# Optimization experiments

Hardware: AMD Instinct MI355X
Metric: run time of the kernel (lower is better)

The kernel has to match this reference:

```python
import jax, jax.numpy as jnp
import numpy as np
from jax import lax

KS = 5            # patch kernel size
STRIDE = 4        # patch stride / scale ratio
SHIFTS = (2, 2)   # roll shifts before patch extraction
SOFTMAX_SCALE = 10.0
MID_CH = 64
BAND_HS = 8


def same_pad(x, k, s):
    """TensorFlow-style SAME padding for kernel k, stride s (NCHW)."""
    H, W = x.shape[-2], x.shape[-1]
    oh, ow = -(-H // s), -(-W // s)
    ph = max(0, (oh - 1) * s + k - H)
    pw = max(0, (ow - 1) * s + k - W)
    return jnp.pad(x, ((0, 0), (0, 0), (ph // 2, ph - ph // 2), (pw // 2, pw - pw // 2)))


def extract_patches(x, k, s, shifts):
    """torch.nn.Unfold equivalent with SAME padding and roll -> [N, L, C, k, k]."""
    x = same_pad(x, k, s)
    x = jnp.roll(x, shifts[0], axis=2)
    x = jnp.roll(x, shifts[1], axis=3)
    p = lax.conv_general_dilated_patches(
        x, (k, k), (s, s), 'VALID', dimension_numbers=('NCHW', 'OIHW', 'NCHW'))
    N, _, Hn, Wn = p.shape
    C = x.shape[1]
    # channel ordering is (C, kh, kw) channel-slowest, matching torch unfold
    return p.reshape(N, C, k, k, Hn * Wn).transpose(0, 4, 1, 2, 3)


def conv3(x, w, b):
    """3x3 conv, padding=1, bias + LeakyReLU(0.01) (BasicBlock)."""
    y = lax.conv_general_dilated(x, w, (1, 1), [(1, 1), (1, 1)],
                                 dimension_numbers=('NCHW', 'OIHW', 'NCHW'))
    return jax.nn.leaky_relu(y + b[None, :, None, None], 0.01)


def setup_inputs() -> dict:
    key = jax.random.key(0)
    ks = jax.random.split(key, 11)
    f32 = jnp.float32
    return {
        'ms':   jax.random.normal(ks[0], (2, BAND_HS, 96, 96), f32),
        'pan':  jax.random.normal(ks[1], (2, 1, 384, 384), f32),
        'pan2': jax.random.normal(ks[2], (2, 1, 96, 96), f32),
        'wq': jax.random.normal(ks[3], (MID_CH, 1, 3, 3), f32) * 0.1,
        'bq': jax.random.normal(ks[4], (MID_CH,), f32) * 0.02,
        'wk': jax.random.normal(ks[5], (MID_CH, 1, 3, 3), f32) * 0.1,
        'bk': jax.random.normal(ks[6], (MID_CH,), f32) * 0.02,
        'wv': jax.random.normal(ks[7], (BAND_HS, BAND_HS, 3, 3), f32) * 0.1,
        'bv': jax.random.normal(ks[8], (BAND_HS,), f32) * 0.02,
        'wr': jax.random.normal(ks[9], (BAND_HS, BAND_HS, 3, 3), f32) * 0.1,
        'br': jax.random.normal(ks[10], (BAND_HS,), f32) * 0.02,
    }


def reference(ms, pan, pan2, wq, bq, wk, bk, wv, bv, wr, br):
    k_fea = conv3(pan2, wk, bk)                       # [N, mid, h, w]
    q_fea = conv3(pan, wq, bq)                        # [N, mid, H, W]
    v_fea = conv3(ms, wv, bv)                         # [N, band, h, w]

    k_patch = extract_patches(k_fea, KS, STRIDE, SHIFTS)  # [N, L, mid, ks, ks]
    v_patch = extract_patches(v_fea, KS, STRIDE, SHIFTS)  # [N, L, band, ks, ks]

    def attend(q, kp, vp):
        # q: [mid, H, W]; kp: [L, mid, ks, ks]; vp: [L, band, ks, ks]
        norms = jnp.sqrt(jnp.sum(kp * kp, axis=(1, 2, 3)))      # per-patch L2 norms
        k0 = kp / jnp.max(norms)                                # global-max normalization
        q0 = same_pad(q[None], KS, STRIDE)                      # [1, mid, Hp, Wp]
        scores = lax.conv_general_dilated(
            q0, k0, (STRIDE, STRIDE), 'VALID',
            dimension_numbers=('NCHW', 'OIHW', 'NCHW'))          # [1, L, H', W']
        attn = jax.nn.softmax(scores * SOFTMAX_SCALE, axis=1)
        # conv_transpose2d(attn, vp, stride) == dilated conv with flipped, transposed kernel
        wT = jnp.flip(vp, (2, 3)).transpose(1, 0, 2, 3)          # [band, L, ks, ks]
        out = lax.conv_general_dilated(
            attn, wT, (1, 1), [(KS - 1, KS - 1)] * 2,
            lhs_dilation=(STRIDE, STRIDE),
            dimension_numbers=('NCHW', 'OIHW', 'NCHW'))          # [1, band, Ho, Wo]
        return out[0] / 6.0

    res = jax.vmap(attend)(q_fea, k_patch, v_patch)   # [N, band, Ho, Wo]
    return conv3(res, wr, br)
```

## Files before the change

kernel.cpp:

```cpp
#include <hip/hip_runtime.h>
#include <math.h>


typedef _Float16 f16;
typedef _Float16 f16x8 __attribute__((ext_vector_type(8)));
typedef float f32x4 __attribute__((ext_vector_type(4)));

namespace csa {
constexpr int NB   = 2;
constexpr int MID  = 64;
constexpr int BAND = 8;
constexpr int HK   = 96;
constexpr int HQ   = 384;
constexpr int HQP  = 385;
constexpr int XI   = 97;
constexpr int LN   = 24;
constexpr int L    = 576;
constexpr int LP   = 640;
constexpr int PS   = 96 * 96;
constexpr int KDIM = MID * 25;
constexpr int VDIM = BAND * 25;
constexpr int MV   = 256;
constexpr int HO   = 385;
constexpr size_t QPSN = (size_t)4 * HQP * XI * MID;

constexpr size_t align256(size_t x) { return (x + 255) & ~(size_t)255; }
constexpr size_t OFF_QPS  = 0;
constexpr size_t OFF_KCL  = align256(OFF_QPS + (size_t)NB*QPSN*2);
constexpr size_t OFF_VFEA = align256(OFF_KCL + (size_t)NB*HK*HK*MID*2);
constexpr size_t OFF_N2   = align256(OFF_VFEA + (size_t)NB*BAND*HK*HK*4);
constexpr size_t OFF_SC   = align256(OFF_N2   + (size_t)NB*L*4);
constexpr size_t OFF_KM   = align256(OFF_SC   + 256);
constexpr size_t OFF_VT   = align256(OFF_KM   + (size_t)NB*LP*KDIM*2);
constexpr size_t OFF_ST   = align256(OFF_VT   + (size_t)NB*MV*L*2);
constexpr size_t OFF_AT   = align256(OFF_ST   + (size_t)NB*PS*LP*4);
constexpr size_t OFF_D    = align256(OFF_AT   + (size_t)NB*PS*L*2);
constexpr size_t OFF_RES  = align256(OFF_D    + (size_t)NB*MV*PS*4);
}
using namespace csa;

__global__ __launch_bounds__(256) void csa_convq_ps(
    const float* __restrict__ in, const float* __restrict__ w,
    const float* __restrict__ b, f16* __restrict__ out) {
  int id = blockIdx.x * 256 + threadIdx.x;
  int total = NB * 4 * HQP * XI;
  if (id >= total) return;
  int xi = id % XI;
  int t = id / XI;
  int yp = t % HQP;
  t /= HQP;
  int f = t % 4;
  int n = t / 4;
  int xp = 4 * xi + f;
  f16* op = out + (size_t)id * MID;
  if (yp >= HQ || xp >= HQ) {
    f16x8 z = {0, 0, 0, 0, 0, 0, 0, 0};
#pragma unroll
    for (int c8 = 0; c8 < 8; ++c8) *(f16x8*)(op + c8 * 8) = z;
    return;
  }
  const float* ip = in + (size_t)n * HQ * HQ;
  float p[9];
#pragma unroll
  for (int dy = 0; dy < 3; ++dy)
#pragma unroll
    for (int dx = 0; dx < 3; ++dx) {
      int yy = yp + dy - 1, xx = xp + dx - 1;
      p[dy * 3 + dx] = (yy >= 0 && yy < HQ && xx >= 0 && xx < HQ)
                           ? ip[(size_t)yy * HQ + xx] : 0.f;
    }
#pragma unroll
  for (int c8 = 0; c8 < 8; ++c8) {
    f16x8 o;
#pragma unroll
    for (int e = 0; e < 8; ++e) {
      int co = c8 * 8 + e;
      float acc = b[co];
#pragma unroll
      for (int k = 0; k < 9; ++k) acc = fmaf(p[k], w[co * 9 + k], acc);
      o[e] = (f16)(acc > 0.f ? acc : 0.01f * acc);
    }
    *(f16x8*)(op + c8 * 8) = o;
  }
}

__global__ __launch_bounds__(256) void csa_conv_cl(
    const float* __restrict__ in, const float* __restrict__ w,
    const float* __restrict__ b, f16* __restrict__ out, int H) {
  int id = blockIdx.x * 256 + threadIdx.x;
  int total = NB * H * H;
  if (id >= total) return;
  int x = id % H;
  int t = id / H;
  int y = t % H;
  int n = t / H;
  f16* op = out + (size_t)id * MID;
  const float* ip = in + (size_t)n * H * H;
  float p[9];
#pragma unroll
  for (int dy = 0; dy < 3; ++dy)
#pragma unroll
    for (int dx = 0; dx < 3; ++dx) {
      int yy = y + dy - 1, xx = x + dx - 1;
      p[dy * 3 + dx] = (yy >= 0 && yy < H && xx >= 0 && xx < H)
                           ? ip[(size_t)yy * H + xx] : 0.f;
    }
#pragma unroll
  for (int c8 = 0; c8 < 8; ++c8) {
    f16x8 o;
#pragma unroll
    for (int e = 0; e < 8; ++e) {
      int co = c8 * 8 + e;
      float acc = b[co];
#pragma unroll
      for (int k = 0; k < 9; ++k) acc = fmaf(p[k], w[co * 9 + k], acc);
      o[e] = (f16)(acc > 0.f ? acc : 0.01f * acc);
    }
    *(f16x8*)(op + c8 * 8) = o;
  }
}

__global__ __launch_bounds__(256) void csa_conv3_8x8(
    const float* __restrict__ in, const float* __restrict__ w,
    const float* __restrict__ b, float* __restrict__ out, int H, int W) {
  int id = blockIdx.x * 256 + threadIdx.x;
  int total = NB * H * W;
  if (id >= total) return;
  int x = id % W;
  int t = id / W;
  int y = t % H;
  int n = t / H;
  const float* ip = in + (size_t)n * BAND * H * W;
  float p[BAND][9];
#pragma unroll
  for (int ci = 0; ci < BAND; ++ci)
#pragma unroll
    for (int dy = 0; dy < 3; ++dy)
#pragma unroll
      for (int dx = 0; dx < 3; ++dx) {
        int yy = y + dy - 1, xx = x + dx - 1;
        p[ci][dy * 3 + dx] = (yy >= 0 && yy < H && xx >= 0 && xx < W)
                                 ? ip[((size_t)ci * H + yy) * W + xx] : 0.f;
      }
  float* op = out + ((size_t)n * BAND * H + y) * W + x;
  for (int co = 0; co < BAND; ++co) {
    float acc = b[co];
#pragma unroll
    for (int ci = 0; ci < BAND; ++ci)
#pragma unroll
      for (int k = 0; k < 9; ++k)
        acc = fmaf(p[ci][k], w[(co * BAND + ci) * 9 + k], acc);
    acc = acc > 0.f ? acc : 0.01f * acc;
    op[(size_t)co * H * W] = acc;
  }
}

__global__ __launch_bounds__(256) void csa_build_patches(
    const f16* __restrict__ kcl, const float* __restrict__ v_fea,
    f16* __restrict__ Kmat, f16* __restrict__ Vt, float* __restrict__ n2) {
  int blk = blockIdx.x;
  int n = blk / LP;
  int l = blk % LP;
  int tid = threadIdx.x;
  f16* krow = Kmat + ((size_t)n * LP + l) * KDIM;
  if (l >= L) {
    f16x8 z = {0, 0, 0, 0, 0, 0, 0, 0};
    for (int ch = tid; ch < 200; ch += 256) *(f16x8*)(krow + ch * 8) = z;
    return;
  }
  int i = l / LN, j = l % LN;
  const f16* kn = kcl + (size_t)n * HK * HK * MID;
  float ss = 0.f;
  for (int ch = tid; ch < 200; ch += 256) {
    int khkw = ch >> 3;
    int c0 = (ch & 7) * 8;
    int kh = khkw / 5, kw = khkw % 5;
    int r = (4 * i + kh + 95) % 97;
    int cc = (4 * j + kw + 95) % 97;
    f16x8 v = {0, 0, 0, 0, 0, 0, 0, 0};
    if (r < HK && cc < HK)
      v = *(const f16x8*)(kn + ((size_t)r * HK + cc) * MID + c0);
#pragma unroll
    for (int e = 0; e < 8; ++e) {
      float fv = (float)v[e];
      ss += fv * fv;
    }
    *(f16x8*)(krow + ch * 8) = v;
  }
  for (int m = tid; m < MV; m += 256) {
    float v = 0.f;
    if (m < VDIM) {
      int kw = m % 5;
      int t = m / 5;
      int kh = t % 5;
      int c = t / 5;
      int r = (4 * i + kh + 95) % 97;
      int cc = (4 * j + kw + 95) % 97;
      v = (r < HK && cc < HK)
              ? v_fea[(((size_t)n * BAND + c) * HK + r) * HK + cc] : 0.f;
    }
    Vt[((size_t)n * MV + m) * L + l] = (f16)v;
  }
  __shared__ float red[256];
  red[tid] = ss;
  __syncthreads();
  for (int s = 128; s > 0; s >>= 1) {
    if (tid < s) red[tid] += red[tid + s];
    __syncthreads();
  }
  if (tid == 0) n2[n * L + l] = red[0];
}

__global__ __launch_bounds__(256) void csa_max_scale(
    const float* __restrict__ n2, float* __restrict__ scale) {
  int n = blockIdx.x;
  int tid = threadIdx.x;
  float m = 0.f;
  for (int l = tid; l < L; l += 256) m = fmaxf(m, n2[n * L + l]);
  __shared__ float red[256];
  red[tid] = m;
  __syncthreads();
  for (int s = 128; s > 0; s >>= 1) {
    if (tid < s) red[tid] = fmaxf(red[tid], red[tid + s]);
    __syncthreads();
  }
  if (tid == 0) scale[n] = 10.f / sqrtf(red[0]);
}

__device__ __forceinline__ void gl_lds16(const f16* g, f16* s) {
  __builtin_amdgcn_global_load_lds(
      (const __attribute__((address_space(1))) void*)g,
      (__attribute__((address_space(3))) void*)s, 16, 0, 0);
}

__global__ __launch_bounds__(256) void csa_gemm1(
    const f16* __restrict__ qps, const f16* __restrict__ Km,
    float* __restrict__ C) {
  __shared__ __attribute__((aligned(16))) f16 As[4096];
  __shared__ __attribute__((aligned(16))) f16 Bs[4096];
  const int tid = threadIdx.x;
  const int w = tid >> 6;
  const int l = tid & 63;
  const int q = l >> 4;
  const int r = l & 15;
  const int nb = blockIdx.z;
  qps += (size_t)nb * QPSN;
  Km += (size_t)nb * LP * KDIM;
  C += (size_t)nb * (size_t)PS * LP;
  const int bm = blockIdx.y * 128;
  const int bn = blockIdx.x * 128;
  const int wm = (w >> 1) * 64;
  const int wn = (w & 1) * 64;

  f32x4 acc[4][4];
#pragma unroll
  for (int i = 0; i < 4; ++i)
#pragma unroll
    for (int j = 0; j < 4; ++j) {
      f32x4 z = {0.f, 0.f, 0.f, 0.f};
      acc[i][j] = z;
    }

  const int pg0 = bm + w * 16;
  const int y0 = pg0 / 96, x0 = pg0 % 96;
  const int pg1 = pg0 + 64;
  const int y1 = pg1 / 96, x1 = pg1 % 96;
  const int la = r * MID + q * 8;

  const f16* gb0 = Km + (size_t)(bn + w * 16 + r) * KDIM + q * 8;
  const f16* gb1 = gb0 + (size_t)64 * KDIM;
  f16* lA0 = As + w * 512;
  f16* lA1 = As + 2048 + w * 512;
  f16* lB0 = Bs + w * 512;
  f16* lB1 = Bs + 2048 + w * 512;
  const int am = (w >> 1) * 4;
  const int bnn = (w & 1) * 4;

  int t = 0;
  for (int kh = 0; kh < 5; ++kh) {
    for (int kw = 0; kw < 5; ++kw) {
      const size_t u0 =
          (((size_t)(kw & 3) * HQP + (4 * y0 + kh)) * XI + x0 + (kw >> 2)) * MID;
      const size_t u1 =
          (((size_t)(kw & 3) * HQP + (4 * y1 + kh)) * XI + x1 + (kw >> 2)) * MID;
#pragma unroll
      for (int half = 0; half < 2; ++half, ++t) {
        const size_t oA = (size_t)half * 32 + la;
        const size_t oB = (size_t)t * 32;
        gl_lds16(qps + u0 + oA, lA0);
        gl_lds16(qps + u1 + oA, lA1);
        gl_lds16(gb0 + oB, lB0);
        gl_lds16(gb1 + oB, lB1);
        __syncthreads();
        f16x8 af[4], bf[4];
#pragma unroll
        for (int u = 0; u < 4; ++u) {
          af[u] = *(const f16x8*)&As[(am + u) * 512 + q * 128 + r * 8];
          bf[u] = *(const f16x8*)&Bs[(bnn + u) * 512 + q * 128 + r * 8];
        }
#pragma unroll
        for (int i = 0; i < 4; ++i)
#pragma unroll
          for (int j = 0; j < 4; ++j)
            acc[i][j] = __builtin_amdgcn_mfma_f32_16x16x32_f16(af[i], bf[j],
                                                               acc[i][j], 0, 0, 0);
        __syncthreads();
      }
    }
  }
  const int cn = bn + wn + r;
#pragma unroll
  for (int i = 0; i < 4; ++i) {
    int rm = bm + wm + i * 16 + q * 4;
#pragma unroll
    for (int j = 0; j < 4; ++j)
#pragma unroll
      for (int rr = 0; rr < 4; ++rr)
        C[(size_t)(rm + rr) * LP + cn + j * 16] = acc[i][j][rr];
  }
}

__global__ __launch_bounds__(256) void csa_gemm_f16(
    const f16* __restrict__ A, const f16* __restrict__ Bt,
    float* __restrict__ C, int M, int N, int K,
    size_t strideA, size_t strideB, size_t strideC) {
  __shared__ __attribute__((aligned(16))) f16 As[4096];
  __shared__ __attribute__((aligned(16))) f16 Bs[4096];
  const int tid = threadIdx.x;
  const int w = tid >> 6;
  const int l = tid & 63;
  const int q = l >> 4;
  const int r = l & 15;
  const int nb = blockIdx.z;
  A += (size_t)nb * strideA;
  Bt += (size_t)nb * strideB;
  C += (size_t)nb * strideC;
  const int bm = blockIdx.y * 128;
  const int bn = blockIdx.x * 128;
  const int wm = (w >> 1) * 64;
  const int wn = (w & 1) * 64;

  f32x4 acc[4][4];
#pragma unroll
  for (int i = 0; i < 4; ++i)
#pragma unroll
    for (int j = 0; j < 4; ++j) {
      f32x4 z = {0.f, 0.f, 0.f, 0.f};
      acc[i][j] = z;
    }

  const f16* ga0 = A + (size_t)(bm + w * 16 + r) * K + q * 8;
  const f16* ga1 = ga0 + (size_t)64 * K;
  const f16* gb0 = Bt + (size_t)(bn + w * 16 + r) * K + q * 8;
  const f16* gb1 = gb0 + (size_t)64 * K;
  f16* lA0 = As + w * 512;
  f16* lA1 = As + 2048 + w * 512;
  f16* lB0 = Bs + w * 512;
  f16* lB1 = Bs + 2048 + w * 512;
  const int am = (w >> 1) * 4;
  const int bnn = (w & 1) * 4;

  for (int k0 = 0; k0 < K; k0 += 32) {
    gl_lds16(ga0 + k0, lA0);
    gl_lds16(ga1 + k0, lA1);
    gl_lds16(gb0 + k0, lB0);
    gl_lds16(gb1 + k0, lB1);
    __syncthreads();
    f16x8 af[4], bf[4];
#pragma unroll
    for (int u = 0; u < 4; ++u) {
      af[u] = *(const f16x8*)&As[(am + u) * 512 + q * 128 + r * 8];
      bf[u] = *(const f16x8*)&Bs[(bnn + u) * 512 + q * 128 + r * 8];
    }
#pragma unroll
    for (int i = 0; i < 4; ++i)
#pragma unroll
      for (int j = 0; j < 4; ++j)
        acc[i][j] =
            __builtin_amdgcn_mfma_f32_16x16x32_f16(af[i], bf[j], acc[i][j], 0, 0, 0);
    __syncthreads();
  }

  const int cn = bn + wn + r;
#pragma unroll
  for (int i = 0; i < 4; ++i) {
    int rm = bm + wm + i * 16 + q * 4;
#pragma unroll
    for (int j = 0; j < 4; ++j)
#pragma unroll
      for (int rr = 0; rr < 4; ++rr)
        C[(size_t)(rm + rr) * N + cn + j * 16] = acc[i][j][rr];
  }
}

__global__ __launch_bounds__(256) void csa_softmax(
    const float* __restrict__ scoresT, const float* __restrict__ scale,
    f16* __restrict__ attnT) {
  const int wv = threadIdx.x >> 6;
  const int lane = threadIdx.x & 63;
  const int p = blockIdx.x * 4 + wv;
  const int n = blockIdx.y;
  const float sc = scale[n];
  const float* row = scoresT + ((size_t)n * PS + p) * LP;
  float v[9];
  float m = -1e30f;
#pragma unroll
  for (int j = 0; j < 9; ++j) {
    v[j] = row[lane + j * 64] * sc;
    m = fmaxf(m, v[j]);
  }
#pragma unroll
  for (int off = 32; off > 0; off >>= 1) m = fmaxf(m, __shfl_xor(m, off));
  float e[9], s = 0.f;
#pragma unroll
  for (int j = 0; j < 9; ++j) {
    e[j] = __expf(v[j] - m);
    s += e[j];
  }
#pragma unroll
  for (int off = 32; off > 0; off >>= 1) s += __shfl_xor(s, off);
  const float inv = 1.f / s;
  f16* orow = attnT + ((size_t)n * PS + p) * L;
#pragma unroll
  for (int j = 0; j < 9; ++j) orow[lane + j * 64] = (f16)(e[j] * inv);
}

__global__ __launch_bounds__(256) void csa_gather(
    const float* __restrict__ D, float* __restrict__ res) {
  int id = blockIdx.x * 256 + threadIdx.x;
  if (id >= NB * BAND * HO * HO) return;
  int ox = id % HO;
  int t = id / HO;
  int oy = t % HO;
  t = t / HO;
  int co = t % BAND;
  int n = t / BAND;
  const float* Dn = D + (size_t)n * MV * PS;
  float s = 0.f;
  int kh0 = oy & 3;
  int kw0 = ox & 3;
  for (int kh = kh0; kh < 5; kh += 4) {
    int y = (oy - kh) >> 2;
    if (y < 0 || y >= 96) continue;
    for (int kw = kw0; kw < 5; kw += 4) {
      int x = (ox - kw) >> 2;
      if (x < 0 || x >= 96) continue;
      s += Dn[(size_t)(co * 25 + kh * 5 + kw) * PS + y * 96 + x];
    }
  }
  res[id] = s * (1.f / 6.f);
}

extern "C" void kernel_launch(void* const* d_in, const int* in_sizes, int n_in,
                              void* d_out, int out_size, void* d_ws,
                              size_t ws_size, hipStream_t stream) {
  const float* ms   = (const float*)d_in[0];
  const float* pan  = (const float*)d_in[1];
  const float* pan2 = (const float*)d_in[2];
  const float* wq = (const float*)d_in[3];
  const float* bq = (const float*)d_in[4];
  const float* wk = (const float*)d_in[5];
  const float* bk = (const float*)d_in[6];
  const float* wv = (const float*)d_in[7];
  const float* bv = (const float*)d_in[8];
  const float* wr = (const float*)d_in[9];
  const float* br = (const float*)d_in[10];
  float* out = (float*)d_out;

  char* ws = (char*)d_ws;
  f16*   qps   = (f16*)(ws + OFF_QPS);
  f16*   kcl   = (f16*)(ws + OFF_KCL);
  float* v_fea = (float*)(ws + OFF_VFEA);
  float* n2    = (float*)(ws + OFF_N2);
  float* scale = (float*)(ws + OFF_SC);
  f16*   Kmat  = (f16*)(ws + OFF_KM);
  f16*   Vt    = (f16*)(ws + OFF_VT);
  float* scoT  = (float*)(ws + OFF_ST);
  f16*   attnT = (f16*)(ws + OFF_AT);
  float* Dm    = (float*)(ws + OFF_D);
  float* res   = (float*)(ws + OFF_RES);

  dim3 b256(256);
  csa_convq_ps<<<dim3((NB * 4 * HQP * XI + 255) / 256), b256, 0, stream>>>(
      pan, wq, bq, qps);
  csa_conv_cl<<<dim3((NB * HK * HK + 255) / 256), b256, 0, stream>>>(
      pan2, wk, bk, kcl, HK);
  csa_conv3_8x8<<<dim3((NB * HK * HK + 255) / 256), b256, 0, stream>>>(
      ms, wv, bv, v_fea, HK, HK);
  csa_build_patches<<<dim3(NB * LP), b256, 0, stream>>>(kcl, v_fea, Kmat, Vt,
                                                        n2);
  csa_max_scale<<<dim3(NB), b256, 0, stream>>>(n2, scale);

  csa_gemm1<<<dim3(LP / 128, PS / 128, NB), b256, 0, stream>>>(qps, Kmat,
                                                               scoT);

  csa_softmax<<<dim3(PS / 4, NB), b256, 0, stream>>>(scoT, scale, attnT);

  csa_gemm_f16<<<dim3(PS / 128, MV / 128, NB), b256, 0, stream>>>(
      Vt, attnT, Dm, MV, PS, L,
      (size_t)MV * L, (size_t)PS * L, (size_t)MV * PS);

  csa_gather<<<dim3((NB * BAND * HO * HO + 255) / 256), b256, 0, stream>>>(
      Dm, res);
  csa_conv3_8x8<<<dim3((NB * HO * HO + 255) / 256), b256, 0, stream>>>(
      res, wr, br, out, HO, HO);
}
```

Before: 279.4 us.

## Double GEMM K-step, store D as fp16, fuse gather with output conv

Both GEMM kernels now stage 64 K-elements per barrier pair instead of 32, halving the synchronisations and doubling LDS tiles. The second GEMM writes its result in fp16, halving the traffic for the large intermediate D. The col2im gather and the final 3x3 conv are fused into one tiled kernel that builds the result tile with halo in shared memory, removing the res buffer round trip and one launch. The fp16 D adds rounding error, and the larger LDS footprint may lower occupancy.

```diff
diff --git a/kernel.cpp b/kernel.cpp
--- a/kernel.cpp
+++ b/kernel.cpp
@@ -35,7 +35,6 @@
 constexpr size_t OFF_ST   = align256(OFF_VT   + (size_t)NB*MV*L*2);
 constexpr size_t OFF_AT   = align256(OFF_ST   + (size_t)NB*PS*LP*4);
 constexpr size_t OFF_D    = align256(OFF_AT   + (size_t)NB*PS*L*2);
-constexpr size_t OFF_RES  = align256(OFF_D    + (size_t)NB*MV*PS*4);
 }
 using namespace csa;
 
@@ -236,8 +235,8 @@
 __global__ __launch_bounds__(256) void csa_gemm1(
     const f16* __restrict__ qps, const f16* __restrict__ Km,
     float* __restrict__ C) {
-  __shared__ __attribute__((aligned(16))) f16 As[4096];
-  __shared__ __attribute__((aligned(16))) f16 Bs[4096];
+  __shared__ __attribute__((aligned(16))) f16 As[8192];
+  __shared__ __attribute__((aligned(16))) f16 Bs[8192];
   const int tid = threadIdx.x;
   const int w = tid >> 6;
   const int l = tid & 63;
@@ -269,34 +268,37 @@
 
   const f16* gb0 = Km + (size_t)(bn + w * 16 + r) * KDIM + q * 8;
   const f16* gb1 = gb0 + (size_t)64 * KDIM;
-  f16* lA0 = As + w * 512;
-  f16* lA1 = As + 2048 + w * 512;
-  f16* lB0 = Bs + w * 512;
-  f16* lB1 = Bs + 2048 + w * 512;
+  f16* lA0 = As + w * 1024;
+  f16* lA1 = As + 4096 + w * 1024;
+  f16* lB0 = Bs + w * 1024;
+  f16* lB1 = Bs + 4096 + w * 1024;
   const int am = (w >> 1) * 4;
   const int bnn = (w & 1) * 4;
 
-  int t = 0;
   for (int kh = 0; kh < 5; ++kh) {
+#pragma unroll
     for (int kw = 0; kw < 5; ++kw) {
       const size_t u0 =
-          (((size_t)(kw & 3) * HQP + (4 * y0 + kh)) * XI + x0 + (kw >> 2)) * MID;
+          (((size_t)(kw & 3) * HQP + (4 * y0 + kh)) * XI + x0 + (kw >> 2)) * MID + la;
       const size_t u1 =
-          (((size_t)(kw & 3) * HQP + (4 * y1 + kh)) * XI + x1 + (kw >> 2)) * MID;
-#pragma unroll
-      for (int half = 0; half < 2; ++half, ++t) {
-        const size_t oA = (size_t)half * 32 + la;
-        const size_t oB = (size_t)t * 32;
-        gl_lds16(qps + u0 + oA, lA0);
-        gl_lds16(qps + u1 + oA, lA1);
-        gl_lds16(gb0 + oB, lB0);
-        gl_lds16(gb1 + oB, lB1);
-        __syncthreads();
+          (((size_t)(kw & 3) * HQP + (4 * y1 + kh)) * XI + x1 + (kw >> 2)) * MID + la;
+      const size_t oB = (size_t)(kh * 5 + kw) * 64;
+      gl_lds16(qps + u0, lA0);
+      gl_lds16(qps + u0 + 32, lA0 + 512);
+      gl_lds16(qps + u1, lA1);
+      gl_lds16(qps + u1 + 32, lA1 + 512);
+      gl_lds16(gb0 + oB, lB0);
+      gl_lds16(gb0 + oB + 32, lB0 + 512);
+      gl_lds16(gb1 + oB, lB1);
+      gl_lds16(gb1 + oB + 32, lB1 + 512);
+      __syncthreads();
+#pragma unroll
+      for (int kk = 0; kk < 2; ++kk) {
         f16x8 af[4], bf[4];
 #pragma unroll
         for (int u = 0; u < 4; ++u) {
-          af[u] = *(const f16x8*)&As[(am + u) * 512 + q * 128 + r * 8];
-          bf[u] = *(const f16x8*)&Bs[(bnn + u) * 512 + q * 128 + r * 8];
+          af[u] = *(const f16x8*)&As[(am + u) * 1024 + kk * 512 + q * 128 + r * 8];
+          bf[u] = *(const f16x8*)&Bs[(bnn + u) * 1024 + kk * 512 + q * 128 + r * 8];
         }
 #pragma unroll
         for (int i = 0; i < 4; ++i)
@@ -304,8 +306,8 @@
           for (int j = 0; j < 4; ++j)
             acc[i][j] = __builtin_amdgcn_mfma_f32_16x16x32_f16(af[i], bf[j],
                                                                acc[i][j], 0, 0, 0);
-        __syncthreads();
       }
+      __syncthreads();
     }
   }
   const int cn = bn + wn + r;
@@ -320,12 +322,12 @@
   }
 }
 
-__global__ __launch_bounds__(256) void csa_gemm_f16(
+__global__ __launch_bounds__(256) void csa_gemm2(
     const f16* __restrict__ A, const f16* __restrict__ Bt,
-    float* __restrict__ C, int M, int N, int K,
+    f16* __restrict__ C, int M, int N, int K,
     size_t strideA, size_t strideB, size_t strideC) {
-  __shared__ __attribute__((aligned(16))) f16 As[4096];
-  __shared__ __attribute__((aligned(16))) f16 Bs[4096];
+  __shared__ __attribute__((aligned(16))) f16 As[8192];
+  __shared__ __attribute__((aligned(16))) f16 Bs[8192];
   const int tid = threadIdx.x;
   const int w = tid >> 6;
   const int l = tid & 63;
@@ -353,31 +355,38 @@
   const f16* ga1 = ga0 + (size_t)64 * K;
   const f16* gb0 = Bt + (size_t)(bn + w * 16 + r) * K + q * 8;
   const f16* gb1 = gb0 + (size_t)64 * K;
-  f16* lA0 = As + w * 512;
-  f16* lA1 = As + 2048 + w * 512;
-  f16* lB0 = Bs + w * 512;
-  f16* lB1 = Bs + 2048 + w * 512;
+  f16* lA0 = As + w * 1024;
+  f16* lA1 = As + 4096 + w * 1024;
+  f16* lB0 = Bs + w * 1024;
+  f16* lB1 = Bs + 4096 + w * 1024;
   const int am = (w >> 1) * 4;
   const int bnn = (w & 1) * 4;
 
-  for (int k0 = 0; k0 < K; k0 += 32) {
+  for (int k0 = 0; k0 < K; k0 += 64) {
     gl_lds16(ga0 + k0, lA0);
+    gl_lds16(ga0 + k0 + 32, lA0 + 512);
     gl_lds16(ga1 + k0, lA1);
+    gl_lds16(ga1 + k0 + 32, lA1 + 512);
     gl_lds16(gb0 + k0, lB0);
+    gl_lds16(gb0 + k0 + 32, lB0 + 512);
     gl_lds16(gb1 + k0, lB1);
+    gl_lds16(gb1 + k0 + 32, lB1 + 512);
     __syncthreads();
-    f16x8 af[4], bf[4];
-#pragma unroll
-    for (int u = 0; u < 4; ++u) {
-      af[u] = *(const f16x8*)&As[(am + u) * 512 + q * 128 + r * 8];
-      bf[u] = *(const f16x8*)&Bs[(bnn + u) * 512 + q * 128 + r * 8];
-    }
-#pragma unroll
-    for (int i = 0; i < 4; ++i)
-#pragma unroll
-      for (int j = 0; j < 4; ++j)
-        acc[i][j] =
-            __builtin_amdgcn_mfma_f32_16x16x32_f16(af[i], bf[j], acc[i][j], 0, 0, 0);
+#pragma unroll
+    for (int kk = 0; kk < 2; ++kk) {
+      f16x8 af[4], bf[4];
+#pragma unroll
+      for (int u = 0; u < 4; ++u) {
+        af[u] = *(const f16x8*)&As[(am + u) * 1024 + kk * 512 + q * 128 + r * 8];
+        bf[u] = *(const f16x8*)&Bs[(bnn + u) * 1024 + kk * 512 + q * 128 + r * 8];
+      }
+#pragma unroll
+      for (int i = 0; i < 4; ++i)
+#pragma unroll
+        for (int j = 0; j < 4; ++j)
+          acc[i][j] = __builtin_amdgcn_mfma_f32_16x16x32_f16(af[i], bf[j],
+                                                             acc[i][j], 0, 0, 0);
+    }
     __syncthreads();
   }
 
@@ -389,7 +398,7 @@
     for (int j = 0; j < 4; ++j)
 #pragma unroll
       for (int rr = 0; rr < 4; ++rr)
-        C[(size_t)(rm + rr) * N + cn + j * 16] = acc[i][j][rr];
+        C[(size_t)(rm + rr) * N + cn + j * 16] = (f16)acc[i][j][rr];
   }
 }
 
@@ -425,30 +434,70 @@
   for (int j = 0; j < 9; ++j) orow[lane + j * 64] = (f16)(e[j] * inv);
 }
 
-__global__ __launch_bounds__(256) void csa_gather(
-    const float* __restrict__ D, float* __restrict__ res) {
-  int id = blockIdx.x * 256 + threadIdx.x;
-  if (id >= NB * BAND * HO * HO) return;
-  int ox = id % HO;
-  int t = id / HO;
-  int oy = t % HO;
-  t = t / HO;
-  int co = t % BAND;
-  int n = t / BAND;
-  const float* Dn = D + (size_t)n * MV * PS;
-  float s = 0.f;
-  int kh0 = oy & 3;
-  int kw0 = ox & 3;
-  for (int kh = kh0; kh < 5; kh += 4) {
-    int y = (oy - kh) >> 2;
-    if (y < 0 || y >= 96) continue;
-    for (int kw = kw0; kw < 5; kw += 4) {
-      int x = (ox - kw) >> 2;
-      if (x < 0 || x >= 96) continue;
-      s += Dn[(size_t)(co * 25 + kh * 5 + kw) * PS + y * 96 + x];
-    }
-  }
-  res[id] = s * (1.f / 6.f);
+__global__ __launch_bounds__(256) void csa_out(
+    const f16* __restrict__ D, const float* __restrict__ wr,
+    const float* __restrict__ br, float* __restrict__ out) {
+  __shared__ float resS[8][34 * 35];
+  __shared__ float wrS[576];
+  __shared__ float brS[8];
+  const int tid = threadIdx.x;
+  const int ty0 = blockIdx.y * 32, tx0 = blockIdx.x * 32;
+  const int n = blockIdx.z;
+  for (int i = tid; i < 576; i += 256) wrS[i] = wr[i];
+  if (tid < 8) brS[tid] = br[tid];
+  const f16* Dn = D + (size_t)n * MV * PS;
+  for (int v = tid; v < 8 * 34 * 34; v += 256) {
+    int ci = v / 1156;
+    int rem = v - ci * 1156;
+    int ryi = rem / 34;
+    int rxi = rem - ryi * 34;
+    int ry = ty0 - 1 + ryi;
+    int rx = tx0 - 1 + rxi;
+    float s = 0.f;
+    if (ry >= 0 && ry < HO && rx >= 0 && rx < HO) {
+      int kh0 = ry & 3, kw0 = rx & 3;
+      for (int kh = kh0; kh < 5; kh += 4) {
+        int y = (ry - kh) >> 2;
+        if (y < 0 || y >= 96) continue;
+        for (int kw = kw0; kw < 5; kw += 4) {
+          int x = (rx - kw) >> 2;
+          if (x < 0 || x >= 96) continue;
+          s += (float)Dn[(size_t)(ci * 25 + kh * 5 + kw) * PS + y * 96 + x];
+        }
+      }
+      s *= (1.f / 6.f);
+    }
+    resS[ci][ryi * 35 + rxi] = s;
+  }
+  __syncthreads();
+  for (int pp = tid; pp < 1024; pp += 256) {
+    int py = pp >> 5, px = pp & 31;
+    int oy = ty0 + py, ox = tx0 + px;
+    if (oy >= HO || ox >= HO) continue;
+    float accs[8];
+#pragma unroll
+    for (int co = 0; co < 8; ++co) accs[co] = brS[co];
+#pragma unroll
+    for (int ci = 0; ci < 8; ++ci) {
+      float rv[9];
+#pragma unroll
+      for (int dy = 0; dy < 3; ++dy)
+#pragma unroll
+        for (int dx = 0; dx < 3; ++dx)
+          rv[dy * 3 + dx] = resS[ci][(py + dy) * 35 + (px + dx)];
+#pragma unroll
+      for (int co = 0; co < 8; ++co)
+#pragma unroll
+        for (int k = 0; k < 9; ++k)
+          accs[co] = fmaf(rv[k], wrS[(co * 8 + ci) * 9 + k], accs[co]);
+    }
+#pragma unroll
+    for (int co = 0; co < 8; ++co) {
+      float a = accs[co];
+      a = a > 0.f ? a : 0.01f * a;
+      out[(((size_t)n * BAND + co) * HO + oy) * HO + ox] = a;
+    }
+  }
 }
 
 extern "C" void kernel_launch(void* const* d_in, const int* in_sizes, int n_in,
@@ -477,8 +526,7 @@
   f16*   Vt    = (f16*)(ws + OFF_VT);
   float* scoT  = (float*)(ws + OFF_ST);
   f16*   attnT = (f16*)(ws + OFF_AT);
-  float* Dm    = (float*)(ws + OFF_D);
-  float* res   = (float*)(ws + OFF_RES);
+  f16*   Dm    = (f16*)(ws + OFF_D);
 
   dim3 b256(256);
   csa_convq_ps<<<dim3((NB * 4 * HQP * XI + 255) / 256), b256, 0, stream>>>(
@@ -496,12 +544,10 @@
 
   csa_softmax<<<dim3(PS / 4, NB), b256, 0, stream>>>(scoT, scale, attnT);
 
-  csa_gemm_f16<<<dim3(PS / 128, MV / 128, NB), b256, 0, stream>>>(
+  csa_gemm2<<<dim3(PS / 128, MV / 128, NB), b256, 0, stream>>>(
       Vt, attnT, Dm, MV, PS, L,
       (size_t)MV * L, (size_t)PS * L, (size_t)MV * PS);
 
-  csa_gather<<<dim3((NB * BAND * HO * HO + 255) / 256), b256, 0, stream>>>(
-      Dm, res);
-  csa_conv3_8x8<<<dim3((NB * HO * HO + 255) / 256), b256, 0, stream>>>(
-      res, wr, br, out, HO, HO);
-}
+  csa_out<<<dim3((HO + 31) / 32, (HO + 31) / 32, NB), b256, 0, stream>>>(
+      Dm, wr, br, out);
+}
```

New measurement: 389.2 us. 1.39x slower.
